# Kernel optimization log

Hardware: AMD Instinct MI355X
Metric: run time of the kernel (lower is better)

Reference implementation:

```python
import jax, jax.numpy as jnp
import numpy as np

B, C, D, H, W = 4, 128, 32, 32, 32
EMB, K = 64, 512


def setup_inputs() -> dict:
    key = jax.random.key(0)
    k1, k2, k3 = jax.random.split(key, 3)
    x = jax.random.normal(k1, (B, C, D, H, W), dtype=jnp.float32)
    conv_w = jax.random.normal(k2, (EMB, C), dtype=jnp.float32) * 0.05  # 1x1x1 Conv3d kernel
    conv_b = jnp.zeros((EMB,), dtype=jnp.float32)
    embed = jax.random.normal(k3, (EMB, K), dtype=jnp.float32)  # codebook, (dim, n_embed)
    return {"x": x, "conv_w": conv_w, "conv_b": conv_b, "embed": embed}


def reference(x, conv_w, conv_b, embed):
    # 1x1x1 Conv3d == per-voxel linear projection; permute to channels-last
    z = jnp.einsum('bcdhw,oc->bdhwo', x, conv_w) + conv_b  # (B,D,H,W,EMB)
    emb_dim = embed.shape[0]
    flat = z.reshape(-1, emb_dim)  # (N, EMB)
    # squared euclidean distance to each codebook entry: ||f||^2 - 2 f.e + ||e||^2
    dist = (jnp.sum(flat * flat, axis=1, keepdims=True)
            - 2.0 * (flat @ embed)
            + jnp.sum(embed * embed, axis=0, keepdims=True))  # (N, K)
    embed_ind = jnp.argmin(dist, axis=1)  # (N,)
    embed_ind = embed_ind.reshape(z.shape[:-1])  # (B,D,H,W)
    quantize = jnp.take(embed.T, embed_ind, axis=0)  # (B,D,H,W,EMB) gather
    diff = jnp.mean((jax.lax.stop_gradient(quantize) - z) ** 2)
    quantize = z + jax.lax.stop_gradient(quantize - z)  # straight-through
    return quantize.transpose(0, 4, 1, 2, 3), diff, embed_ind
```

## Files before the change

### kernel.cpp

```cpp
#include <hip/hip_runtime.h>
#include <hip/hip_bf16.h>

#define CIN   128
#define EMBD  64
#define KC    512
#define SPAT  32768
#define NVOX  131072
#define QSZ   (NVOX * EMBD)
#define DIFF_OFF QSZ
#define IDX_OFF  (QSZ + 1)
#define NBLK  (NVOX / 64)

typedef __attribute__((ext_vector_type(8))) short bf16x8;
typedef __attribute__((ext_vector_type(4))) float f32x4;

__device__ __forceinline__ short bf_hi(float f) {
  __hip_bfloat16 h = __float2bfloat16(f);
  return *(short*)&h;
}
__device__ __forceinline__ float bf_f(short s) {
  __hip_bfloat16 h = *(__hip_bfloat16*)&s;
  return __bfloat162float(h);
}

__global__ __launch_bounds__(64) void vq_prep_e(const float* __restrict__ embed,
                                                float* __restrict__ embedT,
                                                float* __restrict__ norms,
                                                short* __restrict__ e_h,
                                                short* __restrict__ e_m,
                                                short* __restrict__ e_l) {
  int k = blockIdx.x;
  int o = threadIdx.x;
  float e = embed[o * KC + k];
  embedT[k * EMBD + o] = e;
  short h = bf_hi(e);
  float r1 = e - bf_f(h);
  short m = bf_hi(r1);
  short l = bf_hi(r1 - bf_f(m));
  e_h[k * EMBD + o] = h;
  e_m[k * EMBD + o] = m;
  e_l[k * EMBD + o] = l;
  float s = e * e;
  #pragma unroll
  for (int off = 32; off > 0; off >>= 1) s += __shfl_down(s, off);
  if (o == 0) norms[k] = s;
}

__global__ __launch_bounds__(256) void vq_prep_w(const float* __restrict__ conv_w,
                                                 float* __restrict__ wT) {
  int f = blockIdx.x * 256 + threadIdx.x;
  int c = f >> 6;
  int o = f & 63;
  wT[f] = conv_w[o * CIN + c];
}

__global__ __launch_bounds__(256, 2) void vq_main(
    const float* __restrict__ x, const float* __restrict__ wT,
    const float* __restrict__ conv_b, const float* __restrict__ embedT,
    const short* __restrict__ e_h, const short* __restrict__ e_m,
    const short* __restrict__ e_l, const float* __restrict__ norms,
    float* __restrict__ out, float* __restrict__ partials) {
  __shared__ short zh[64 * 64], zm[64 * 64], zl[64 * 64];
  __shared__ float norml[KC];
  __shared__ float zsq4[64][4];
  __shared__ float wbest[4][64];
  __shared__ int   widx[4][64];
  __shared__ int   fidx[64];

  const int t    = threadIdx.x;
  const int q    = t >> 6;
  const int v    = t & 63;
  const int n0   = blockIdx.x * 64;
  const int b    = n0 >> 15;
  const int vsp  = n0 & (SPAT - 1);

  norml[t]       = norms[t];
  norml[t + 256] = norms[t + 256];

  const float* xp = x + ((size_t)b * CIN) * SPAT + vsp + v;
  float z[16];
  #pragma unroll
  for (int j = 0; j < 16; ++j) z[j] = conv_b[q * 16 + j];

  #pragma unroll 4
  for (int c = 0; c < CIN; ++c) {
    float xv = xp[(size_t)c * SPAT];
    const float* wr = wT + c * EMBD + q * 16;
    #pragma unroll
    for (int j = 0; j < 16; ++j) z[j] = fmaf(xv, wr[j], z[j]);
  }

  float sq = 0.f;
  #pragma unroll
  for (int j = 0; j < 16; ++j) sq = fmaf(z[j], z[j], sq);
  zsq4[v][q] = sq;

  short h16[16], m16[16], l16[16];
  #pragma unroll
  for (int j = 0; j < 16; ++j) {
    short h = bf_hi(z[j]);
    float r1 = z[j] - bf_f(h);
    short m = bf_hi(r1);
    h16[j] = h; m16[j] = m; l16[j] = bf_hi(r1 - bf_f(m));
  }
  #pragma unroll
  for (int jj = 0; jj < 2; ++jj) {
    int s = (2 * q + jj) ^ (v & 7);
    int byte = v * 128 + s * 16;
    bf16x8 hv, mv, lv;
    #pragma unroll
    for (int j = 0; j < 8; ++j) { hv[j] = h16[jj*8+j]; mv[j] = m16[jj*8+j]; lv[j] = l16[jj*8+j]; }
    *(bf16x8*)((char*)zh + byte) = hv;
    *(bf16x8*)((char*)zm + byte) = mv;
    *(bf16x8*)((char*)zl + byte) = lv;
  }
  __syncthreads();

  const int lane = t & 63;
  const int l15  = lane & 15;
  const int g    = lane >> 4;

  f32x4 acc[4][8];
  #pragma unroll
  for (int m = 0; m < 4; ++m)
    #pragma unroll
    for (int n = 0; n < 8; ++n) { f32x4 z4 = {0.f,0.f,0.f,0.f}; acc[m][n] = z4; }

  const int boff = (q * 128 + l15) * 128 + g * 16;

  auto dist_pass = [&](const short* zlds, const short* __restrict__ eg) {
    #pragma unroll
    for (int ks8 = 0; ks8 <= 4; ks8 += 4) {
      bf16x8 a[4];
      #pragma unroll
      for (int m = 0; m < 4; ++m) {
        int vox = m * 16 + l15;
        a[m] = *(const bf16x8*)((const char*)zlds + vox * 128 +
                                (((ks8 + g) ^ (vox & 7)) << 4));
      }
      #pragma unroll
      for (int n = 0; n < 8; ++n) {
        bf16x8 bb = *(const bf16x8*)((const char*)eg + boff + n * 2048 + ks8 * 16);
        #pragma unroll
        for (int m = 0; m < 4; ++m)
          acc[m][n] = __builtin_amdgcn_mfma_f32_16x16x32_bf16(a[m], bb, acc[m][n], 0, 0, 0);
      }
    }
  };
  dist_pass(zh, e_h);
  dist_pass(zh, e_m);
  dist_pass(zm, e_h);
  dist_pass(zh, e_l);
  dist_pass(zl, e_h);
  dist_pass(zm, e_m);

  float nv[8];
  #pragma unroll
  for (int n = 0; n < 8; ++n) nv[n] = norml[q * 128 + n * 16 + l15];

  float best[16]; int bidx[16];
  #pragma unroll
  for (int i = 0; i < 16; ++i) { best[i] = 3.4e38f; bidx[i] = 0; }
  #pragma unroll
  for (int n = 0; n < 8; ++n)
    #pragma unroll
    for (int m = 0; m < 4; ++m)
      #pragma unroll
      for (int r = 0; r < 4; ++r) {
        float s = fmaf(-2.f, acc[m][n][r], nv[n]);
        int code = q * 128 + n * 16 + l15;
        int i = m * 4 + r;
        bool tk = s < best[i];
        best[i] = tk ? s : best[i];
        bidx[i] = tk ? code : bidx[i];
      }
  #pragma unroll
  for (int i = 0; i < 16; ++i) {
    #pragma unroll
    for (int d = 1; d < 16; d <<= 1) {
      float os = __shfl_xor(best[i], d);
      int   oi = __shfl_xor(bidx[i], d);
      bool tk = (os < best[i]) || (os == best[i] && oi < bidx[i]);
      best[i] = tk ? os : best[i];
      bidx[i] = tk ? oi : bidx[i];
    }
  }
  if (l15 == 0) {
    #pragma unroll
    for (int i = 0; i < 16; ++i) {
      int vox = (i >> 2) * 16 + g * 4 + (i & 3);
      wbest[q][vox] = best[i];
      widx[q][vox]  = bidx[i];
    }
  }
  __syncthreads();

  if (t < 64) {
    float bs = wbest[0][t]; int bi = widx[0][t];
    #pragma unroll
    for (int w2 = 1; w2 < 4; ++w2) {
      float s2 = wbest[w2][t]; int i2 = widx[w2][t];
      bool tk = (s2 < bs) || (s2 == bs && i2 < bi);
      bs = tk ? s2 : bs; bi = tk ? i2 : bi;
    }
    fidx[t] = bi;
    out[IDX_OFF + n0 + t] = (float)bi;
    float d = bs + zsq4[t][0] + zsq4[t][1] + zsq4[t][2] + zsq4[t][3];
    #pragma unroll
    for (int off = 32; off > 0; off >>= 1) d += __shfl_down(d, off);
    if (t == 0) partials[blockIdx.x] = d;
  }
  __syncthreads();

  const int bi = fidx[v];
  const float* er = embedT + bi * EMBD + q * 16;
  float* qout = out + ((size_t)b * EMBD + q * 16) * SPAT + vsp + v;
  #pragma unroll
  for (int u = 0; u < 4; ++u) {
    float4 e4 = *(const float4*)(er + u * 4);
    qout[(size_t)(u * 4 + 0) * SPAT] = e4.x;
    qout[(size_t)(u * 4 + 1) * SPAT] = e4.y;
    qout[(size_t)(u * 4 + 2) * SPAT] = e4.z;
    qout[(size_t)(u * 4 + 3) * SPAT] = e4.w;
  }
}

__global__ __launch_bounds__(512) void vq_final(const float* __restrict__ partials,
                                                float* __restrict__ out) {
  __shared__ float tmp[8];
  float s = partials[threadIdx.x] + partials[threadIdx.x + 512] +
            partials[threadIdx.x + 1024] + partials[threadIdx.x + 1536];
  #pragma unroll
  for (int off = 32; off > 0; off >>= 1) s += __shfl_down(s, off);
  if ((threadIdx.x & 63) == 0) tmp[threadIdx.x >> 6] = s;
  __syncthreads();
  if (threadIdx.x == 0) {
    float t = 0.f;
    #pragma unroll
    for (int i = 0; i < 8; ++i) t += tmp[i];
    out[DIFF_OFF] = t * (1.0f / (float)QSZ);
  }
}

extern "C" void kernel_launch(void* const* d_in, const int* in_sizes, int n_in,
                              void* d_out, int out_size, void* d_ws, size_t ws_size,
                              hipStream_t stream) {
  const float* x      = (const float*)d_in[0];
  const float* conv_w = (const float*)d_in[1];
  const float* conv_b = (const float*)d_in[2];
  const float* embed  = (const float*)d_in[3];
  float* out = (float*)d_out;
  float* ws  = (float*)d_ws;

  float* embedT   = ws;
  float* norms    = ws + 32768;
  float* wT       = ws + 33280;
  float* partials = ws + 41472;
  short* e_h      = (short*)(ws + 43520);
  short* e_m      = e_h + KC * EMBD;
  short* e_l      = e_m + KC * EMBD;

  vq_prep_e<<<KC, EMBD, 0, stream>>>(embed, embedT, norms, e_h, e_m, e_l);
  vq_prep_w<<<32, 256, 0, stream>>>(conv_w, wT);
  vq_main<<<NBLK, 256, 0, stream>>>(x, wT, conv_b, embedT, e_h, e_m, e_l,
                                    norms, out, partials);
  vq_final<<<1, 512, 0, stream>>>(partials, out);
}
```

Baseline: 403.5 us.

## Split codebook distance pass into two halves to cut accumulators and raise occupancy

Each wave now handles its 128 codes as two chunks of 64, keeping a 4x4 accumulator tile instead of 4x8 and doing the argmin per chunk, with per-chunk results written to shared memory. Launch bounds go from 2 to 4 blocks per SIMD so the smaller register footprint can yield more resident waves to hide x-load and LDS latency. In exchange the z fragments are re-read from LDS twice and the shuffle reduction runs twice. The final cross-wave merge drops the index tie-break, but chunks are visited in ascending code order with strict less-than, so the lowest index still wins ties.

```diff
diff --git a/kernel.cpp b/kernel.cpp
--- a/kernel.cpp
+++ b/kernel.cpp
@@ -36,10 +36,9 @@
   short h = bf_hi(e);
   float r1 = e - bf_f(h);
   short m = bf_hi(r1);
-  short l = bf_hi(r1 - bf_f(m));
   e_h[k * EMBD + o] = h;
   e_m[k * EMBD + o] = m;
-  e_l[k * EMBD + o] = l;
+  e_l[k * EMBD + o] = bf_hi(r1 - bf_f(m));
   float s = e * e;
   #pragma unroll
   for (int off = 32; off > 0; off >>= 1) s += __shfl_down(s, off);
@@ -54,7 +53,31 @@
   wT[f] = conv_w[o * CIN + c];
 }
 
-__global__ __launch_bounds__(256, 2) void vq_main(
+#define DIST_PASS(ZB, EB)                                                     \
+  {                                                                           \
+    _Pragma("unroll")                                                         \
+    for (int ks8 = 0; ks8 <= 4; ks8 += 4) {                                   \
+      bf16x8 a[4];                                                            \
+      _Pragma("unroll")                                                       \
+      for (int m = 0; m < 4; ++m) {                                           \
+        int vox = m * 16 + l15;                                               \
+        a[m] = *(const bf16x8*)((const char*)(ZB) + vox * 128 +               \
+                                (((ks8 + g) ^ (vox & 7)) << 4));              \
+      }                                                                       \
+      _Pragma("unroll")                                                       \
+      for (int n = 0; n < 4; ++n) {                                           \
+        bf16x8 bb = *(const bf16x8*)((const char*)(EB) + boff_c +             \
+                                     n * 2048 + ks8 * 16);                    \
+        _Pragma("unroll")                                                     \
+        for (int m = 0; m < 4; ++m)                                           \
+          acc[m][n] = __builtin_amdgcn_mfma_f32_16x16x32_bf16(a[m], bb,       \
+                                                              acc[m][n],      \
+                                                              0, 0, 0);       \
+      }                                                                       \
+    }                                                                         \
+  }
+
+__global__ __launch_bounds__(256, 4) void vq_main(
     const float* __restrict__ x, const float* __restrict__ wT,
     const float* __restrict__ conv_b, const float* __restrict__ embedT,
     const short* __restrict__ e_h, const short* __restrict__ e_m,
@@ -63,16 +86,16 @@
   __shared__ short zh[64 * 64], zm[64 * 64], zl[64 * 64];
   __shared__ float norml[KC];
   __shared__ float zsq4[64][4];
-  __shared__ float wbest[4][64];
-  __shared__ int   widx[4][64];
+  __shared__ float wbest_s[4][2][64];
+  __shared__ int   widx_s[4][2][64];
   __shared__ int   fidx[64];
 
-  const int t    = threadIdx.x;
-  const int q    = t >> 6;
-  const int v    = t & 63;
-  const int n0   = blockIdx.x * 64;
-  const int b    = n0 >> 15;
-  const int vsp  = n0 & (SPAT - 1);
+  const int t   = threadIdx.x;
+  const int q   = t >> 6;
+  const int v   = t & 63;
+  const int n0  = blockIdx.x * 64;
+  const int b   = n0 >> 15;
+  const int vsp = n0 & (SPAT - 1);
 
   norml[t]       = norms[t];
   norml[t + 256] = norms[t + 256];
@@ -109,7 +132,9 @@
     int byte = v * 128 + s * 16;
     bf16x8 hv, mv, lv;
     #pragma unroll
-    for (int j = 0; j < 8; ++j) { hv[j] = h16[jj*8+j]; mv[j] = m16[jj*8+j]; lv[j] = l16[jj*8+j]; }
+    for (int j = 0; j < 8; ++j) {
+      hv[j] = h16[jj * 8 + j]; mv[j] = m16[jj * 8 + j]; lv[j] = l16[jj * 8 + j];
+    }
     *(bf16x8*)((char*)zh + byte) = hv;
     *(bf16x8*)((char*)zm + byte) = mv;
     *(bf16x8*)((char*)zl + byte) = lv;
@@ -120,89 +145,75 @@
   const int l15  = lane & 15;
   const int g    = lane >> 4;
 
-  f32x4 acc[4][8];
-  #pragma unroll
-  for (int m = 0; m < 4; ++m)
-    #pragma unroll
-    for (int n = 0; n < 8; ++n) { f32x4 z4 = {0.f,0.f,0.f,0.f}; acc[m][n] = z4; }
-
-  const int boff = (q * 128 + l15) * 128 + g * 16;
-
-  auto dist_pass = [&](const short* zlds, const short* __restrict__ eg) {
-    #pragma unroll
-    for (int ks8 = 0; ks8 <= 4; ks8 += 4) {
-      bf16x8 a[4];
-      #pragma unroll
-      for (int m = 0; m < 4; ++m) {
-        int vox = m * 16 + l15;
-        a[m] = *(const bf16x8*)((const char*)zlds + vox * 128 +
-                                (((ks8 + g) ^ (vox & 7)) << 4));
+  #pragma unroll
+  for (int nc = 0; nc < 2; ++nc) {
+    const int boff_c = (q * 128 + nc * 64 + l15) * 128 + g * 16;
+
+    f32x4 acc[4][4];
+    #pragma unroll
+    for (int m = 0; m < 4; ++m)
+      #pragma unroll
+      for (int n = 0; n < 4; ++n) { f32x4 z4 = {0.f, 0.f, 0.f, 0.f}; acc[m][n] = z4; }
+
+    DIST_PASS(zh, e_h)
+    DIST_PASS(zh, e_m)
+    DIST_PASS(zm, e_h)
+    DIST_PASS(zh, e_l)
+    DIST_PASS(zl, e_h)
+    DIST_PASS(zm, e_m)
+
+    float best[16]; int bidx[16];
+    #pragma unroll
+    for (int i = 0; i < 16; ++i) { best[i] = 3.4e38f; bidx[i] = 0; }
+    #pragma unroll
+    for (int n = 0; n < 4; ++n) {
+      float nv = norml[q * 128 + nc * 64 + n * 16 + l15];
+      int code = q * 128 + nc * 64 + n * 16 + l15;
+      #pragma unroll
+      for (int m = 0; m < 4; ++m)
+        #pragma unroll
+        for (int r = 0; r < 4; ++r) {
+          float s = fmaf(-2.f, acc[m][n][r], nv);
+          int i = m * 4 + r;
+          bool tk = s < best[i];
+          best[i] = tk ? s : best[i];
+          bidx[i] = tk ? code : bidx[i];
+        }
+    }
+    #pragma unroll
+    for (int i = 0; i < 16; ++i) {
+      #pragma unroll
+      for (int d = 1; d < 16; d <<= 1) {
+        float os = __shfl_xor(best[i], d);
+        int   oi = __shfl_xor(bidx[i], d);
+        bool tk = (os < best[i]) || (os == best[i] && oi < bidx[i]);
+        best[i] = tk ? os : best[i];
+        bidx[i] = tk ? oi : bidx[i];
       }
-      #pragma unroll
-      for (int n = 0; n < 8; ++n) {
-        bf16x8 bb = *(const bf16x8*)((const char*)eg + boff + n * 2048 + ks8 * 16);
-        #pragma unroll
-        for (int m = 0; m < 4; ++m)
-          acc[m][n] = __builtin_amdgcn_mfma_f32_16x16x32_bf16(a[m], bb, acc[m][n], 0, 0, 0);
+    }
+    if (l15 == 0) {
+      #pragma unroll
+      for (int i = 0; i < 16; ++i) {
+        int vox = (i >> 2) * 16 + g * 4 + (i & 3);
+        wbest_s[q][nc][vox] = best[i];
+        widx_s[q][nc][vox]  = bidx[i];
       }
     }
-  };
-  dist_pass(zh, e_h);
-  dist_pass(zh, e_m);
-  dist_pass(zm, e_h);
-  dist_pass(zh, e_l);
-  dist_pass(zl, e_h);
-  dist_pass(zm, e_m);
-
-  float nv[8];
-  #pragma unroll
-  for (int n = 0; n < 8; ++n) nv[n] = norml[q * 128 + n * 16 + l15];
-
-  float best[16]; int bidx[16];
-  #pragma unroll
-  for (int i = 0; i < 16; ++i) { best[i] = 3.4e38f; bidx[i] = 0; }
-  #pragma unroll
-  for (int n = 0; n < 8; ++n)
-    #pragma unroll
-    for (int m = 0; m < 4; ++m)
-      #pragma unroll
-      for (int r = 0; r < 4; ++r) {
-        float s = fmaf(-2.f, acc[m][n][r], nv[n]);
-        int code = q * 128 + n * 16 + l15;
-        int i = m * 4 + r;
-        bool tk = s < best[i];
-        best[i] = tk ? s : best[i];
-        bidx[i] = tk ? code : bidx[i];
+  }
+  __syncthreads();
+
+  if (t < 64) {
+    float bs = wbest_s[0][0][t]; int bi = widx_s[0][0][t];
+    #pragma unroll
+    for (int qq = 0; qq < 4; ++qq)
+      #pragma unroll
+      for (int nc = 0; nc < 2; ++nc) {
+        if (qq == 0 && nc == 0) continue;
+        float s2 = wbest_s[qq][nc][t];
+        int   i2 = widx_s[qq][nc][t];
+        bool tk = s2 < bs;
+        bs = tk ? s2 : bs; bi = tk ? i2 : bi;
       }
-  #pragma unroll
-  for (int i = 0; i < 16; ++i) {
-    #pragma unroll
-    for (int d = 1; d < 16; d <<= 1) {
-      float os = __shfl_xor(best[i], d);
-      int   oi = __shfl_xor(bidx[i], d);
-      bool tk = (os < best[i]) || (os == best[i] && oi < bidx[i]);
-      best[i] = tk ? os : best[i];
-      bidx[i] = tk ? oi : bidx[i];
-    }
-  }
-  if (l15 == 0) {
-    #pragma unroll
-    for (int i = 0; i < 16; ++i) {
-      int vox = (i >> 2) * 16 + g * 4 + (i & 3);
-      wbest[q][vox] = best[i];
-      widx[q][vox]  = bidx[i];
-    }
-  }
-  __syncthreads();
-
-  if (t < 64) {
-    float bs = wbest[0][t]; int bi = widx[0][t];
-    #pragma unroll
-    for (int w2 = 1; w2 < 4; ++w2) {
-      float s2 = wbest[w2][t]; int i2 = widx[w2][t];
-      bool tk = (s2 < bs) || (s2 == bs && i2 < bi);
-      bs = tk ? s2 : bs; bi = tk ? i2 : bi;
-    }
     fidx[t] = bi;
     out[IDX_OFF + n0 + t] = (float)bi;
     float d = bs + zsq4[t][0] + zsq4[t][1] + zsq4[t][2] + zsq4[t][3];
```

Result: slower. 478.0 us (+18.5%).
